# Performance work log

Hardware: AMD Instinct MI355X
Metric: run time of the kernel (lower is better)

The kernel has to match this reference:

```python
import jax, jax.numpy as jnp
import numpy as np

TARGET_MAIN_CONTRIBUTION = 0.6
CONTRIB_LOSS_COEF = 0.01
TOP_K = 2
NEG_INF = -1e9


def _gat(x, adj, W1, a1s, a1d, W2, a2s, a2d):
    """Dense 2-layer GAT (pyGAT style): multi-head concat + ELU, then one output head.
    x: [B,S,Fin], adj: [B,S,S], W1: [H,Fin,Fh], a1s/a1d: [H,Fh], W2: [H*Fh,Fout], a2s/a2d: [Fout]."""
    mask = adj > 0  # [B,S,S]
    h = jnp.einsum('bsf,hfo->bhso', x, W1)                      # [B,H,S,Fh]
    es = jnp.einsum('bhso,ho->bhs', h, a1s)
    ed = jnp.einsum('bhso,ho->bhs', h, a1d)
    e = jax.nn.leaky_relu(es[:, :, :, None] + ed[:, :, None, :], 0.2)  # [B,H,S,S]
    att = jax.nn.softmax(jnp.where(mask[:, None], e, NEG_INF), axis=-1)
    h1 = jax.nn.elu(jnp.einsum('bhst,bhto->bhso', att, h))      # [B,H,S,Fh]
    B, H, S, Fh = h1.shape
    h1 = h1.transpose(0, 2, 1, 3).reshape(B, S, H * Fh)         # concat heads
    h2 = h1 @ W2                                                # [B,S,Fout]
    e2 = jax.nn.leaky_relu((h2 @ a2s)[:, :, None] + (h2 @ a2d)[:, None, :], 0.2)
    att2 = jax.nn.softmax(jnp.where(mask, e2, NEG_INF), axis=-1)
    return jnp.einsum('bst,bto->bso', att2, h2)


def setup_inputs() -> dict:
    B, S, D, H, Hd, E = 4, 1024, 256, 6, 64, 3
    key = jax.random.key(0)
    ks = jax.random.split(key, 20)
    feature = jax.random.normal(ks[0], (B, S, D), dtype=jnp.float32)
    # sparse-ish binary adjacency with self-loops
    adj = (jax.random.uniform(ks[1], (B, S, S)) < 0.05).astype(jnp.float32)
    adj = jnp.maximum(adj, jnp.eye(S, dtype=jnp.float32)[None])
    p = lambda k, shape: jax.random.normal(k, shape, dtype=jnp.float32) * 0.1
    return {
        'feature': feature, 'adj': adj,
        'main_W1': p(ks[2], (H, D, Hd)), 'main_a1s': p(ks[3], (H, Hd)), 'main_a1d': p(ks[4], (H, Hd)),
        'main_W2': p(ks[5], (H * Hd, D)), 'main_a2s': p(ks[6], (D,)), 'main_a2d': p(ks[7], (D,)),
        'dep_W1': p(ks[8], (E, H, D, Hd)), 'dep_a1s': p(ks[9], (E, H, Hd)), 'dep_a1d': p(ks[10], (E, H, Hd)),
        'dep_W2': p(ks[11], (E, H * Hd, D)), 'dep_a2s': p(ks[12], (E, D)), 'dep_a2d': p(ks[13], (E, D)),
        'router_W': p(ks[14], (D, E)),
        'blend_W': p(ks[15], (D, D)), 'blend_b': jnp.zeros((D,), dtype=jnp.float32),
        'doc_num': 4, 'sect_num': 32,
    }


def reference(feature, adj, main_W1, main_a1s, main_a1d, main_W2, main_a2s, main_a2d,
              dep_W1, dep_a1s, dep_a1d, dep_W2, dep_a2s, dep_a2d,
              router_W, blend_W, blend_b, doc_num, sect_num):
    B, S, D = feature.shape
    E = router_W.shape[1]
    # main expert on full graph
    main_output = _gat(feature, adj, main_W1, main_a1s, main_a1d, main_W2, main_a2s, main_a2d)
    # per-expert adjacency views (zero out columns by node type)
    col = jnp.arange(S)
    sent_cols = (col < S - sect_num - doc_num).astype(adj.dtype)
    sect_cols = ((col >= S - sect_num - doc_num) & (col < S - doc_num)).astype(adj.dtype)
    doc_cols = (col >= S - doc_num).astype(adj.dtype)
    adj_stack = jnp.stack([adj * sent_cols, adj * sect_cols, adj * doc_cols])  # [E,B,S,S]
    # fixed top-k router
    x_flat = feature.reshape(-1, D)
    gate_probs = jax.nn.softmax(x_flat @ router_W, axis=-1)      # [B*S,E]
    _, top_idx = jax.lax.top_k(gate_probs, TOP_K)                # [B*S,k]
    routing_mask = jax.nn.one_hot(top_idx, E, dtype=feature.dtype).sum(axis=-2)  # [B*S,E] binary
    routing_mask = routing_mask.reshape(B, S, E)
    mask_e = routing_mask.transpose(2, 0, 1)[..., None]          # [E,B,S,1]
    # deputy experts: masked input, masked output, accumulate
    x_e = feature[None] * mask_e                                 # [E,B,S,D]
    dep_out = jax.vmap(_gat)(x_e, adj_stack, dep_W1, dep_a1s, dep_a1d, dep_W2, dep_a2s, dep_a2d)
    deputy_output = (dep_out * mask_e).sum(axis=0)               # [B,S,D]
    # blend gate
    blend_weight = jax.nn.sigmoid(feature @ blend_W + blend_b)
    final_output = blend_weight * main_output + (1.0 - blend_weight) * deputy_output
    main_contribution = blend_weight.mean()
    contribution_loss = jnp.abs(main_contribution - TARGET_MAIN_CONTRIBUTION) * CONTRIB_LOSS_COEF
    return final_output, contribution_loss, main_contribution
```

## Files before the change

kernel.cpp:

```cpp
#include <hip/hip_runtime.h>
#include <math.h>

#define B 4
#define S 1024
#define D 256
#define H 6
#define HD 64
#define NE 3
#define HHD 384
#define ROWS (B*S)
#define MAXN 128
#define PLN ((size_t)ROWS*64)

typedef __attribute__((ext_vector_type(8))) short bf8_t;
typedef __attribute__((ext_vector_type(4))) float f32x4;

__device__ __forceinline__ float leaky(float x){ return x > 0.f ? x : 0.2f*x; }

__device__ __forceinline__ unsigned short f2bf(float f){
    union { float f; unsigned int u; } v; v.f = f;
    unsigned int u = v.u;
    return (unsigned short)((u + 0x7FFFu + ((u >> 16) & 1u)) >> 16);
}
__device__ __forceinline__ float bf2f(unsigned short h){
    union { unsigned int u; float f; } v; v.u = ((unsigned int)h) << 16;
    return v.f;
}
__device__ __forceinline__ float blo(unsigned int u){
    union { unsigned int u; float f; } v; v.u = u << 16; return v.f;
}
__device__ __forceinline__ float bhi(unsigned int u){
    union { unsigned int u; float f; } v; v.u = u & 0xffff0000u; return v.f;
}
__device__ __forceinline__ float i2f(int t){
    union { int i; float f; } v; v.i = t; return v.f;
}
__device__ __forceinline__ int f2i(float f){
    union { float f; int i; } v; v.f = f; return v.i;
}
__device__ __forceinline__ unsigned int pk2(float lo, float hi){
    return (unsigned)f2bf(lo) | ((unsigned)f2bf(hi) << 16);
}

struct P {
    const float *feature, *adj;
    const float *main_W1, *dep_W1, *main_W2, *dep_W2, *blend_W, *router_W;
    const int *doc_p, *sect_p;
    const float *main_a1s, *main_a1d, *dep_a1s, *dep_a1d;
    const float *main_a2s, *main_a2d, *dep_a2s, *dep_a2d;
    const float *blend_b;
    unsigned short *featbf; short *nbr; int4 *nbc;
    unsigned short *w1nk, *w2nk, *bwt;
    float *es8, *ed8, *gatebuf;
    unsigned int *htp;
    unsigned short *h2n4, *h1c4;
    float *f2s4, *f2d4, *meanV1p, *meanV2, *sumBuf, *rmask;
    float *outp;
};

#define PB_CONV   1024
#define PB_NBR    1024
#define PB_W1     1536
#define PB_W2     1536
#define PB_BW      256
#define PB_ZERO    177
#define PB_ROUTER 1024
#define PB_TOTAL  (PB_CONV + PB_NBR + PB_W1 + PB_W2 + PB_BW + PB_ZERO + PB_ROUTER)
#define NZERO     45088

__global__ __launch_bounds__(256) void prep_kernel(P pp)
{
    int blk = blockIdx.x, tid = threadIdx.x;
    if (blk < PB_CONV){
        int idx = blk*256 + tid;
        float4 v = ((const float4*)pp.feature)[idx];
        ushort4 o;
        o.x = f2bf(v.x); o.y = f2bf(v.y); o.z = f2bf(v.z); o.w = f2bf(v.w);
        ((ushort4*)pp.featbf)[idx] = o;
        return;
    }
    blk -= PB_CONV;
    if (blk < PB_NBR){
        int wave = tid >> 6, lane = tid & 63;
        int row = blk*4 + wave;
        int b1 = S - *pp.sect_p - *pp.doc_p;
        int b2 = S - *pp.doc_p;
        const float* ar = pp.adj + (size_t)row*S + lane*16;
        float a[16];
        #pragma unroll
        for (int q = 0; q < 4; q++){
            float4 v = ((const float4*)ar)[q];
            a[q*4+0] = v.x; a[q*4+1] = v.y; a[q*4+2] = v.z; a[q*4+3] = v.w;
        }
        int t0 = lane*16;
        int k = 0, c1 = 0, c2 = 0;
        #pragma unroll
        for (int i = 0; i < 16; i++){
            if (a[i] > 0.f){
                k++;
                int t = t0 + i;
                if (t < b1) c1++;
                if (t < b2) c2++;
            }
        }
        int inc = k;
        #pragma unroll
        for (int d = 1; d < 64; d <<= 1){
            int u = __shfl_up(inc, d);
            if (lane >= d) inc += u;
        }
        int off = inc - k;
        int total = __shfl(inc, 63);
        int o = row*MAXN + off;
        #pragma unroll
        for (int i = 0; i < 16; i++){
            if (a[i] > 0.f) pp.nbr[o++] = (short)(t0 + i);
        }
        for (int d = 32; d; d >>= 1){
            c1 += __shfl_down(c1, d);
            c2 += __shfl_down(c2, d);
        }
        if (lane == 0) pp.nbc[row] = make_int4(total, c1, c2, 0);
        return;
    }
    blk -= PB_NBR;
    if (blk < PB_W1){
        int e = blk / 384;
        int idx = (blk - e*384)*256 + tid;
        const float* src = (e == 0) ? pp.main_W1 : pp.dep_W1 + (size_t)(e-1)*H*D*HD;
        int n = idx >> 8, k = idx & 255;
        int h = n >> 6, o = n & 63;
        pp.w1nk[(size_t)e*HHD*D + idx] = f2bf(src[(h*D + k)*HD + o]);
        return;
    }
    blk -= PB_W1;
    if (blk < PB_W2){
        int g = blk*256 + tid;
        int e = g / (D*HHD);
        int rem = g - e*(D*HHD);
        int n = rem / HHD, k = rem - n*HHD;
        const float* src = (e == 0) ? pp.main_W2 : pp.dep_W2 + (size_t)(e-1)*HHD*D;
        pp.w2nk[g] = f2bf(src[k*D + n]);
        return;
    }
    blk -= PB_W2;
    if (blk < PB_BW){
        int col = blk, k = tid;
        pp.bwt[col*D + k] = f2bf(pp.blend_W[k*D + col]);
        return;
    }
    blk -= PB_BW;
    if (blk < PB_ZERO){
        int idx = blk*256 + tid;
        if (idx < NZERO) pp.f2s4[idx] = 0.f;
        return;
    }
    blk -= PB_ZERO;
    {
        int wave = tid >> 6, lane = tid & 63;
        int row = blk*4 + wave;
        float4 xv = ((const float4*)(pp.feature + (size_t)row*D))[lane];
        int f = lane*4;
        float xa[4] = {xv.x, xv.y, xv.z, xv.w};
        float p0 = 0.f, p1 = 0.f, p2 = 0.f;
        #pragma unroll
        for (int j = 0; j < 4; j++){
            p0 += xa[j]*pp.router_W[(f+j)*NE + 0];
            p1 += xa[j]*pp.router_W[(f+j)*NE + 1];
            p2 += xa[j]*pp.router_W[(f+j)*NE + 2];
        }
        for (int off = 32; off; off >>= 1){
            p0 += __shfl_down(p0, off);
            p1 += __shfl_down(p1, off);
            p2 += __shfl_down(p2, off);
        }
        if (lane == 0){
            float p[3] = {p0, p1, p2};
            int ex = 0;
            for (int e = 1; e < NE; e++) if (p[e] <= p[ex]) ex = e;
            for (int e = 0; e < NE; e++) pp.rmask[e*ROWS + row] = (e == ex) ? 0.f : 1.f;
        }
    }
}

__global__ __launch_bounds__(256, 4) void gemm1_kernel(P pp)
{
    __shared__ __align__(16) char smem[17408];
    float (*ep)[2][64][17] = (float (*)[2][64][17])smem;
    unsigned int (*tile)[68] = (unsigned int (*)[68])smem;
    int tid = threadIdx.x, wave = tid >> 6, lane = tid & 63;
    int quad = lane >> 4, l16 = lane & 15;
    int e = blockIdx.z;
    int n0 = blockIdx.y*64;
    f32x4 z4 = {0.f,0.f,0.f,0.f};
    bf8_t bz = {0,0,0,0,0,0,0,0};

    if (e == 4){
        if (blockIdx.x >= 2) return;
        int m0 = blockIdx.x*128;
        const unsigned short* arow0 = pp.bwt + (size_t)(m0 + wave*16 + l16)*D + quad*8;
        const unsigned short* arow1 = arow0 + (size_t)64*D;
        const unsigned short* brow[4];
        #pragma unroll
        for (int j = 0; j < 4; j++)
            brow[j] = pp.featbf + (size_t)(n0 + j*16 + l16)*D + quad*8;
        f32x4 acc[8] = {z4, z4, z4, z4, z4, z4, z4, z4};
        bf8_t a0F = *(const bf8_t*)(arow0);
        bf8_t a1F = *(const bf8_t*)(arow1);
        bf8_t bF[4];
        #pragma unroll
        for (int j = 0; j < 4; j++) bF[j] = *(const bf8_t*)(brow[j]);
        #pragma unroll
        for (int it = 0; it < D/32; it++){
            bf8_t a0C = a0F, a1C = a1F;
            bf8_t bC[4] = {bF[0], bF[1], bF[2], bF[3]};
            if (it + 1 < D/32){
                int kn = (it + 1)*32;
                a0F = *(const bf8_t*)(arow0 + kn);
                a1F = *(const bf8_t*)(arow1 + kn);
                #pragma unroll
                for (int j = 0; j < 4; j++) bF[j] = *(const bf8_t*)(brow[j] + kn);
            }
            #pragma unroll
            for (int j = 0; j < 4; j++){
                acc[j]   = __builtin_amdgcn_mfma_f32_16x16x32_bf16(a0C, bC[j], acc[j],   0, 0, 0);
                acc[4+j] = __builtin_amdgcn_mfma_f32_16x16x32_bf16(a1C, bC[j], acc[4+j], 0, 0, 0);
            }
        }
        int mbase0 = m0 + wave*16 + quad*4;
        int mbase1 = mbase0 + 64;
        float bias0[4], bias1[4];
        #pragma unroll
        for (int r = 0; r < 4; r++){ bias0[r] = pp.blend_b[mbase0 + r]; bias1[r] = pp.blend_b[mbase1 + r]; }
        float lsum = 0.f;
        #pragma unroll
        for (int j = 0; j < 4; j++){
            int rown = n0 + j*16 + l16;
            f32x4 st0, st1;
            #pragma unroll
            for (int r = 0; r < 4; r++){
                float g0 = 1.f/(1.f + __expf(-(acc[j][r] + bias0[r])));
                float g1 = 1.f/(1.f + __expf(-(acc[4+j][r] + bias1[r])));
                lsum += g0 + g1;
                st0[r] = g0; st1[r] = g1;
            }
            *(f32x4*)(pp.gatebuf + (size_t)rown*D + mbase0) = st0;
            *(f32x4*)(pp.gatebuf + (size_t)rown*D + mbase1) = st1;
        }
        float* redp = (float*)smem;
        redp[tid] = lsum;
        __syncthreads();
        for (int sft = 128; sft; sft >>= 1){
            if (tid < sft) redp[tid] += redp[tid + sft];
            __syncthreads();
        }
        if (tid == 0) atomicAdd(pp.sumBuf, redp[0]);
        return;
    }

    int p = blockIdx.x;
    int m0 = p*128;
    const unsigned short* arow0 = pp.w1nk + (size_t)e*HHD*D + (size_t)(m0 + wave*16 + l16)*D + quad*8;
    const unsigned short* arow1 = arow0 + (size_t)64*D;
    const unsigned short* brow[4];
    bool zr[4];
    #pragma unroll
    for (int j = 0; j < 4; j++){
        int n = n0 + j*16 + l16;
        brow[j] = pp.featbf + (size_t)n*D + quad*8;
        zr[j] = (e > 0) ? (pp.rmask[(size_t)(e-1)*ROWS + n] == 0.f) : false;
    }
    f32x4 acc[8] = {z4, z4, z4, z4, z4, z4, z4, z4};
    bf8_t a0F = *(const bf8_t*)(arow0);
    bf8_t a1F = *(const bf8_t*)(arow1);
    bf8_t bF[4];
    #pragma unroll
    for (int j = 0; j < 4; j++) bF[j] = zr[j] ? bz : *(const bf8_t*)(brow[j]);
    #pragma unroll
    for (int it = 0; it < D/32; it++){
        bf8_t a0C = a0F, a1C = a1F;
        bf8_t bC[4] = {bF[0], bF[1], bF[2], bF[3]};
        if (it + 1 < D/32){
            int kn = (it + 1)*32;
            a0F = *(const bf8_t*)(arow0 + kn);
            a1F = *(const bf8_t*)(arow1 + kn);
            #pragma unroll
            for (int j = 0; j < 4; j++) bF[j] = zr[j] ? bz : *(const bf8_t*)(brow[j] + kn);
        }
        #pragma unroll
        for (int j = 0; j < 4; j++){
            acc[j]   = __builtin_amdgcn_mfma_f32_16x16x32_bf16(a0C, bC[j], acc[j],   0, 0, 0);
            acc[4+j] = __builtin_amdgcn_mfma_f32_16x16x32_bf16(a1C, bC[j], acc[4+j], 0, 0, 0);
        }
    }
    int b = n0 >> 10;
    int mbase0 = m0 + wave*16 + quad*4;
    int mbase1 = mbase0 + 64;
    int obase = wave*16 + quad*4;
    int h0 = p*2, h1 = p*2 + 1;
    const float* a1sp = (e == 0) ? pp.main_a1s : pp.dep_a1s + (size_t)(e-1)*H*HD;
    const float* a1dp = (e == 0) ? pp.main_a1d : pp.dep_a1d + (size_t)(e-1)*H*HD;
    float s0v[4], d0v[4], s1v[4], d1v[4];
    #pragma unroll
    for (int r = 0; r < 4; r++){
        s0v[r] = a1sp[mbase0 + r]; d0v[r] = a1dp[mbase0 + r];
        s1v[r] = a1sp[mbase1 + r]; d1v[r] = a1dp[mbase1 + r];
    }
    #pragma unroll
    for (int j = 0; j < 4; j++){
        float ps0 = 0.f, pd0 = 0.f, ps1 = 0.f, pd1 = 0.f;
        #pragma unroll
        for (int r = 0; r < 4; r++){
            ps0 += acc[j][r]*s0v[r];   pd0 += acc[j][r]*d0v[r];
            ps1 += acc[4+j][r]*s1v[r]; pd1 += acc[4+j][r]*d1v[r];
        }
        ep[0][0][j*16 + l16][wave*4 + quad] = ps0;
        ep[0][1][j*16 + l16][wave*4 + quad] = pd0;
        ep[1][0][j*16 + l16][wave*4 + quad] = ps1;
        ep[1][1][j*16 + l16][wave*4 + quad] = pd1;
    }
    float* mvb = pp.meanV1p + ((size_t)e*B + b)*512;
    #pragma unroll
    for (int r = 0; r < 4; r++){
        float cm0 = acc[0][r] + acc[1][r] + acc[2][r] + acc[3][r];
        float cm1 = acc[4][r] + acc[5][r] + acc[6][r] + acc[7][r];
        for (int off = 8; off; off >>= 1){
            cm0 += __shfl_down(cm0, off, 16);
            cm1 += __shfl_down(cm1, off, 16);
        }
        if (l16 == 0){
            atomicAdd(mvb + (obase + r)*8 + h0, cm0*(1.f/(float)S));
            atomicAdd(mvb + (obase + r)*8 + h1, cm1*(1.f/(float)S));
        }
    }
    __syncthreads();
    {
        int hh = tid >> 7, arr = (tid >> 6) & 1, sl = tid & 63;
        float sum = 0.f;
        #pragma unroll
        for (int i = 0; i < 16; i++) sum += ep[hh][arr][sl][i];
        int n = n0 + sl;
        float* dst = arr ? pp.ed8 : pp.es8;
        dst[(((size_t)e*B + (n >> 10))*S + (n & 1023))*8 + (p*2 + hh)] = sum;
    }
    __syncthreads();
    #pragma unroll
    for (int j = 0; j < 4; j++){
        int rloc = j*16 + l16;
        tile[rloc][obase + 0] = pk2(acc[j][0], acc[4+j][0]);
        tile[rloc][obase + 1] = pk2(acc[j][1], acc[4+j][1]);
        tile[rloc][obase + 2] = pk2(acc[j][2], acc[4+j][2]);
        tile[rloc][obase + 3] = pk2(acc[j][3], acc[4+j][3]);
    }
    __syncthreads();
    {
        unsigned int* plane = pp.htp + (size_t)(e*3 + p)*PLN;
        int o4 = (tid & 15)*4;
        int rsub = tid >> 4;
        #pragma unroll
        for (int pass = 0; pass < 4; pass++){
            int rloc = pass*16 + rsub;
            uint4 v = *(const uint4*)&tile[rloc][o4];
            *(uint4*)(plane + (size_t)(n0 + rloc)*64 + o4) = v;
        }
    }
}

__global__ __launch_bounds__(256) void a1_kernel(P pp)
{
    __shared__ f32x4 wMa[MAXN], wMb[MAXN], wDa[MAXN], wDb[MAXN];
    __shared__ f32x4 paccA[4][64], paccB[4][64];
    __shared__ float pdenM[2][6];
    __shared__ float pdenD[2][3][6];
    int tid = threadIdx.x, wave = tid >> 6, lane = tid & 63;
    int s = blockIdx.x, b = blockIdx.y;
    int row = b*S + s;
    int4 c = pp.nbc[row];
    const short* nl = pp.nbr + (size_t)row*MAXN;

    if (wave < 2){
        const float* esp = pp.es8 + ((size_t)b*S + s)*8;
        f32x4 eslo = *(const f32x4*)esp;
        f32x4 eshi = *(const f32x4*)(esp + 4);
        float esv[6] = {eslo[0], eslo[1], eslo[2], eslo[3], eshi[0], eshi[1]};
        const float* edb = pp.ed8 + (size_t)b*S*8;
        int i = wave*64 + lane;
        float w[6] = {0,0,0,0,0,0};
        if (i < c.x){
            int t = nl[i];
            const float* epn = edb + (size_t)t*8;
            f32x4 d0 = *(const f32x4*)epn;
            f32x4 d1 = *(const f32x4*)(epn + 4);
            float edv[6] = {d0[0], d0[1], d0[2], d0[3], d1[0], d1[1]};
            #pragma unroll
            for (int h = 0; h < 6; h++) w[h] = __expf(leaky(esv[h] + edv[h]));
            f32x4 ra = {w[0], w[1], w[2], w[3]};
            f32x4 rb = {w[4], w[5], i2f(t), 0.f};
            wMa[i] = ra; wMb[i] = rb;
        }
        #pragma unroll
        for (int h = 0; h < 6; h++){
            float x = w[h];
            for (int o2 = 32; o2; o2 >>= 1) x += __shfl_down(x, o2);
            if (lane == 0) pdenM[wave][h] = x;
        }
    } else {
        int i = (wave - 2)*64 + lane;
        int tg = (i < c.y) ? 1 : ((i < c.z) ? 2 : 3);
        float w[6] = {0,0,0,0,0,0};
        if (i < c.x){
            int t = nl[i];
            const float* esp = pp.es8 + (((size_t)tg*B + b)*S + s)*8;
            f32x4 eslo = *(const f32x4*)esp;
            f32x4 eshi = *(const f32x4*)(esp + 4);
            const float* epn = pp.ed8 + (((size_t)tg*B + b)*S + (size_t)t)*8;
            f32x4 d0 = *(const f32x4*)epn;
            f32x4 d1 = *(const f32x4*)(epn + 4);
            float es6[6] = {eslo[0], eslo[1], eslo[2], eslo[3], eshi[0], eshi[1]};
            float ed6[6] = {d0[0], d0[1], d0[2], d0[3], d1[0], d1[1]};
            #pragma unroll
            for (int h = 0; h < 6; h++) w[h] = __expf(leaky(es6[h] + ed6[h]));
            float zf = (pp.rmask[(size_t)(tg-1)*ROWS + (size_t)b*S + t] == 0.f) ? 1.f : 0.f;
            f32x4 ra = {w[0], w[1], w[2], w[3]};
            f32x4 rb = {w[4], w[5], zf, 0.f};
            wDa[i] = ra; wDb[i] = rb;
        }
        #pragma unroll
        for (int g = 1; g <= 3; g++){
            #pragma unroll
            for (int h = 0; h < 6; h++){
                float x = (tg == g) ? w[h] : 0.f;
                for (int o2 = 32; o2; o2 >>= 1) x += __shfl_down(x, o2);
                if (lane == 0) pdenD[wave-2][g-1][h] = x;
            }
        }
    }
    __syncthreads();

    const unsigned int* Vm = pp.htp + (size_t)b*S*64 + lane;
    float accM[6] = {0,0,0,0,0,0};
    int rlo[3] = {0, c.y, c.z};
    int rhi[3] = {c.y, c.z, c.x};
    for (int rg = 0; rg < 3; rg++){
        const unsigned int* Vd = pp.htp + (size_t)(rg+1)*3*PLN + (size_t)b*S*64 + lane;
        float accD[6] = {0,0,0,0,0,0};
        #pragma unroll 2
        for (int j = rlo[rg] + wave; j < rhi[rg]; j += 4){
            f32x4 ma = wMa[j], mb = wMb[j];
            f32x4 da = wDa[j], db = wDb[j];
            size_t toff = (size_t)f2i(mb[2])*64;
            unsigned int u0 = Vm[toff];
            unsigned int u1 = Vm[toff + PLN];
            unsigned int u2 = Vm[toff + 2*PLN];
            accM[0] += ma[0]*blo(u0); accM[1] += ma[1]*bhi(u0);
            accM[2] += ma[2]*blo(u1); accM[3] += ma[3]*bhi(u1);
            accM[4] += mb[0]*blo(u2); accM[5] += mb[1]*bhi(u2);
            if (db[2] == 0.f){
                unsigned int d0 = Vd[toff];
                unsigned int d1 = Vd[toff + PLN];
                unsigned int d2 = Vd[toff + 2*PLN];
                accD[0] += da[0]*blo(d0); accD[1] += da[1]*bhi(d0);
                accD[2] += da[2]*blo(d1); accD[3] += da[3]*bhi(d1);
                accD[4] += db[0]*blo(d2); accD[5] += db[1]*bhi(d2);
            }
        }
        {
            f32x4 pa = {accD[0], accD[1], accD[2], accD[3]};
            f32x4 pb = {accD[4], accD[5], 0.f, 0.f};
            paccA[wave][lane] = pa; paccB[wave][lane] = pb;
        }
        __syncthreads();
        if (wave == 0){
            unsigned short* outp = pp.h1c4 + ((size_t)(rg+1)*ROWS + row)*HHD;
            bool has = rhi[rg] > rlo[rg];
            const float* mv = pp.meanV1p + ((size_t)(rg+1)*B + b)*512 + lane*8;
            f32x4 q0 = paccA[0][lane], q1 = paccA[1][lane], q2 = paccA[2][lane], q3 = paccA[3][lane];
            f32x4 r0 = paccB[0][lane], r1 = paccB[1][lane], r2 = paccB[2][lane], r3 = paccB[3][lane];
            float sum6[6];
            sum6[0] = q0[0]+q1[0]+q2[0]+q3[0];
            sum6[1] = q0[1]+q1[1]+q2[1]+q3[1];
            sum6[2] = q0[2]+q1[2]+q2[2]+q3[2];
            sum6[3] = q0[3]+q1[3]+q2[3]+q3[3];
            sum6[4] = r0[0]+r1[0]+r2[0]+r3[0];
            sum6[5] = r0[1]+r1[1]+r2[1]+r3[1];
            #pragma unroll
            for (int h = 0; h < 6; h++){
                float den = pdenD[0][rg][h] + pdenD[1][rg][h];
                float v = has ? sum6[h]/den : mv[h];
                v = v > 0.f ? v : __expf(v) - 1.f;
                outp[h*64 + lane] = f2bf(v);
            }
        }
        __syncthreads();
    }
    {
        f32x4 pa = {accM[0], accM[1], accM[2], accM[3]};
        f32x4 pb = {accM[4], accM[5], 0.f, 0.f};
        paccA[wave][lane] = pa; paccB[wave][lane] = pb;
    }
    __syncthreads();
    if (wave == 0){
        unsigned short* outp = pp.h1c4 + (size_t)row*HHD;
        f32x4 q0 = paccA[0][lane], q1 = paccA[1][lane], q2 = paccA[2][lane], q3 = paccA[3][lane];
        f32x4 r0 = paccB[0][lane], r1 = paccB[1][lane], r2 = paccB[2][lane], r3 = paccB[3][lane];
        float sum6[6];
        sum6[0] = q0[0]+q1[0]+q2[0]+q3[0];
        sum6[1] = q0[1]+q1[1]+q2[1]+q3[1];
        sum6[2] = q0[2]+q1[2]+q2[2]+q3[2];
        sum6[3] = q0[3]+q1[3]+q2[3]+q3[3];
        sum6[4] = r0[0]+r1[0]+r2[0]+r3[0];
        sum6[5] = r0[1]+r1[1]+r2[1]+r3[1];
        #pragma unroll
        for (int h = 0; h < 6; h++){
            float den = pdenM[0][h] + pdenM[1][h];
            float v = sum6[h]/den;
            v = v > 0.f ? v : __expf(v) - 1.f;
            outp[h*64 + lane] = f2bf(v);
        }
    }
}

__global__ __launch_bounds__(256, 4) void gemm2_kernel(P pp)
{
    __shared__ float ep[2][2][64][17];
    int tid = threadIdx.x, wave = tid >> 6, lane = tid & 63;
    int quad = lane >> 4, l16 = lane & 15;
    int e = blockIdx.z;
    int m0 = blockIdx.x*128;
    int n0 = blockIdx.y*64;
    f32x4 z4 = {0.f,0.f,0.f,0.f};
    const unsigned short* arow0 = pp.w2nk + (size_t)e*D*HHD + (size_t)(m0 + wave*16 + l16)*HHD + quad*8;
    const unsigned short* arow1 = arow0 + (size_t)64*HHD;
    const unsigned short* brow[4];
    #pragma unroll
    for (int j = 0; j < 4; j++)
        brow[j] = pp.h1c4 + (size_t)e*ROWS*HHD + (size_t)(n0 + j*16 + l16)*HHD + quad*8;
    f32x4 acc[8] = {z4, z4, z4, z4, z4, z4, z4, z4};
    bf8_t a0F = *(const bf8_t*)(arow0);
    bf8_t a1F = *(const bf8_t*)(arow1);
    bf8_t bF[4];
    #pragma unroll
    for (int j = 0; j < 4; j++) bF[j] = *(const bf8_t*)(brow[j]);
    #pragma unroll
    for (int it = 0; it < HHD/32; it++){
        bf8_t a0C = a0F, a1C = a1F;
        bf8_t bC[4] = {bF[0], bF[1], bF[2], bF[3]};
        if (it + 1 < HHD/32){
            int kn = (it + 1)*32;
            a0F = *(const bf8_t*)(arow0 + kn);
            a1F = *(const bf8_t*)(arow1 + kn);
            #pragma unroll
            for (int j = 0; j < 4; j++) bF[j] = *(const bf8_t*)(brow[j] + kn);
        }
        #pragma unroll
        for (int j = 0; j < 4; j++){
            acc[j]   = __builtin_amdgcn_mfma_f32_16x16x32_bf16(a0C, bC[j], acc[j],   0, 0, 0);
            acc[4+j] = __builtin_amdgcn_mfma_f32_16x16x32_bf16(a1C, bC[j], acc[4+j], 0, 0, 0);
        }
    }
    int b = n0 >> 10;
    int mbase0 = m0 + wave*16 + quad*4;
    int mbase1 = mbase0 + 64;
    #pragma unroll
    for (int j = 0; j < 4; j++){
        int row = n0 + j*16 + l16;
        ushort4 o0, o1;
        o0.x = f2bf(acc[j][0]);   o0.y = f2bf(acc[j][1]);
        o0.z = f2bf(acc[j][2]);   o0.w = f2bf(acc[j][3]);
        o1.x = f2bf(acc[4+j][0]); o1.y = f2bf(acc[4+j][1]);
        o1.z = f2bf(acc[4+j][2]); o1.w = f2bf(acc[4+j][3]);
        *(ushort4*)(pp.h2n4 + ((size_t)e*ROWS + row)*D + mbase0) = o0;
        *(ushort4*)(pp.h2n4 + ((size_t)e*ROWS + row)*D + mbase1) = o1;
    }
    const float* a2sp = (e == 0) ? pp.main_a2s : pp.dep_a2s + (size_t)(e-1)*D;
    const float* a2dp = (e == 0) ? pp.main_a2d : pp.dep_a2d + (size_t)(e-1)*D;
    float s0v[4], d0v[4], s1v[4], d1v[4];
    #pragma unroll
    for (int r = 0; r < 4; r++){
        s0v[r] = a2sp[mbase0 + r]; d0v[r] = a2dp[mbase0 + r];
        s1v[r] = a2sp[mbase1 + r]; d1v[r] = a2dp[mbase1 + r];
    }
    #pragma unroll
    for (int j = 0; j < 4; j++){
        float ps0 = 0.f, pd0 = 0.f, ps1 = 0.f, pd1 = 0.f;
        #pragma unroll
        for (int r = 0; r < 4; r++){
            ps0 += acc[j][r]*s0v[r];   pd0 += acc[j][r]*d0v[r];
            ps1 += acc[4+j][r]*s1v[r]; pd1 += acc[4+j][r]*d1v[r];
        }
        ep[0][0][j*16 + l16][wave*4 + quad] = ps0;
        ep[0][1][j*16 + l16][wave*4 + quad] = pd0;
        ep[1][0][j*16 + l16][wave*4 + quad] = ps1;
        ep[1][1][j*16 + l16][wave*4 + quad] = pd1;
    }
    #pragma unroll
    for (int r = 0; r < 4; r++){
        float cm0 = acc[0][r] + acc[1][r] + acc[2][r] + acc[3][r];
        float cm1 = acc[4][r] + acc[5][r] + acc[6][r] + acc[7][r];
        for (int off = 8; off; off >>= 1){
            cm0 += __shfl_down(cm0, off, 16);
            cm1 += __shfl_down(cm1, off, 16);
        }
        if (l16 == 0){
            atomicAdd(pp.meanV2 + ((size_t)e*B + b)*D + mbase0 + r, cm0*(1.f/(float)S));
            atomicAdd(pp.meanV2 + ((size_t)e*B + b)*D + mbase1 + r, cm1*(1.f/(float)S));
        }
    }
    __syncthreads();
    {
        int hh = tid >> 7, arr = (tid >> 6) & 1, sl = tid & 63;
        float sum = 0.f;
        #pragma unroll
        for (int i = 0; i < 16; i++) sum += ep[hh][arr][sl][i];
        int n = n0 + sl;
        float* dst = arr ? pp.f2d4 : pp.f2s4;
        atomicAdd(dst + (size_t)e*ROWS + n, sum);
    }
}

__global__ __launch_bounds__(256) void a2_kernel(P pp)
{
    __shared__ float2 wrec0[MAXN];
    __shared__ float2 wrec1[MAXN];
    __shared__ float pacc[3][256];
    __shared__ float pden[4][4];
    int tid = threadIdx.x;
    int wave = tid >> 6, lane = tid & 63;
    int s = blockIdx.x, b = blockIdx.y;
    int row = b*S + s;
    int4 c = pp.nbc[row];
    float rm0 = pp.rmask[row], rm1 = pp.rmask[ROWS + row], rm2 = pp.rmask[2*ROWS + row];
    const short* nl = pp.nbr + (size_t)row*MAXN;
    if (wave < 2){
        int i = wave*64 + lane;
        float w = 0.f;
        if (i < c.x){
            int t = nl[i];
            float fs = pp.f2s4[row];
            w = __expf(leaky(fs + pp.f2d4[(size_t)b*S + t]));
            float2 r; r.x = w; r.y = i2f(t);
            wrec0[i] = r;
        }
        float dsum = w;
        for (int o2 = 32; o2; o2 >>= 1) dsum += __shfl_down(dsum, o2);
        if (lane == 0) pden[wave][0] = dsum;
    } else {
        int i = (wave - 2)*64 + lane;
        float w = 0.f, d1 = 0.f, d2 = 0.f, d3 = 0.f;
        if (i < c.x){
            int t = nl[i];
            int tag = (i < c.y) ? 1 : ((i < c.z) ? 2 : 3);
            float act = (tag == 1) ? rm0 : ((tag == 2) ? rm1 : rm2);
            if (act != 0.f){
                float fs = pp.f2s4[(size_t)tag*ROWS + row];
                w = __expf(leaky(fs + pp.f2d4[(size_t)tag*ROWS + (size_t)b*S + t]));
            }
            float2 r; r.x = w; r.y = i2f(t);
            wrec1[i] = r;
            if (tag == 1) d1 = w; else if (tag == 2) d2 = w; else d3 = w;
        }
        for (int o2 = 32; o2; o2 >>= 1){
            d1 += __shfl_down(d1, o2);
            d2 += __shfl_down(d2, o2);
            d3 += __shfl_down(d3, o2);
        }
        if (lane == 0){ pden[wave][1] = d1; pden[wave][2] = d2; pden[wave][3] = d3; }
    }
    __syncthreads();
    float acc[4] = {0.f, 0.f, 0.f, 0.f};
    if (wave < 2){
        float inv = 1.f/(pden[0][0] + pden[1][0]);
        const unsigned short* V = pp.h2n4 + (size_t)b*S*D;
        #pragma unroll 4
        for (int j = wave; j < c.x; j += 2){
            float2 r = wrec0[j];
            float wv = r.x*inv;
            int t = f2i(r.y);
            const unsigned short* vp = V + (size_t)t*D + lane*4;
            uint2 dv = *(const uint2*)vp;
            acc[0] += wv*blo(dv.x); acc[1] += wv*bhi(dv.x);
            acc[2] += wv*blo(dv.y); acc[3] += wv*bhi(dv.y);
        }
    } else {
        int rlo[3] = {0, c.y, c.z};
        int rhi[3] = {c.y, c.z, c.x};
        float ract[3] = {rm0, rm1, rm2};
        for (int rg = 0; rg < 3; rg++){
            if (ract[rg] == 0.f || rhi[rg] <= rlo[rg]) continue;
            float inv = 1.f/(pden[2][rg+1] + pden[3][rg+1]);
            const unsigned short* V = pp.h2n4 + ((size_t)(rg+1)*ROWS + (size_t)b*S)*D;
            #pragma unroll 4
            for (int j = rlo[rg] + (wave - 2); j < rhi[rg]; j += 2){
                float2 r = wrec1[j];
                float wv = r.x*inv;
                int t = f2i(r.y);
                const unsigned short* vp = V + (size_t)t*D + lane*4;
                uint2 dv = *(const uint2*)vp;
                acc[0] += wv*blo(dv.x); acc[1] += wv*bhi(dv.x);
                acc[2] += wv*blo(dv.y); acc[3] += wv*bhi(dv.y);
            }
        }
    }
    if (wave >= 1){
        #pragma unroll
        for (int q = 0; q < 4; q++) pacc[wave-1][lane*4 + q] = acc[q];
    }
    __syncthreads();
    if (wave == 0){
        float4 g4 = *(const float4*)(pp.gatebuf + (size_t)row*D + lane*4);
        float dep_mv[4] = {0.f, 0.f, 0.f, 0.f};
        if (rm0 != 0.f && c.y == 0){
            float4 mv = *(const float4*)(pp.meanV2 + ((size_t)1*B + b)*D + lane*4);
            dep_mv[0] += mv.x; dep_mv[1] += mv.y; dep_mv[2] += mv.z; dep_mv[3] += mv.w;
        }
        if (rm1 != 0.f && c.z == c.y){
            float4 mv = *(const float4*)(pp.meanV2 + ((size_t)2*B + b)*D + lane*4);
            dep_mv[0] += mv.x; dep_mv[1] += mv.y; dep_mv[2] += mv.z; dep_mv[3] += mv.w;
        }
        if (rm2 != 0.f && c.x == c.z){
            float4 mv = *(const float4*)(pp.meanV2 + ((size_t)3*B + b)*D + lane*4);
            dep_mv[0] += mv.x; dep_mv[1] += mv.y; dep_mv[2] += mv.z; dep_mv[3] += mv.w;
        }
        float g[4] = {g4.x, g4.y, g4.z, g4.w};
        float4 o;
        float* op = &o.x;
        #pragma unroll
        for (int q = 0; q < 4; q++){
            int col = lane*4 + q;
            float a0 = acc[q] + pacc[0][col];
            float dep = pacc[1][col] + pacc[2][col] + dep_mv[q];
            op[q] = g[q]*a0 + (1.f - g[q])*dep;
        }
        *(float4*)(pp.outp + (size_t)row*D + lane*4) = o;
    }
    if (blockIdx.x == 0 && blockIdx.y == 0 && tid == 0){
        float mc = pp.sumBuf[0] / (float)(ROWS*D);
        pp.outp[ROWS*D]     = fabsf(mc - 0.6f)*0.01f;
        pp.outp[ROWS*D + 1] = mc;
    }
}

extern "C" void kernel_launch(void* const* d_in, const int* in_sizes, int n_in,
                              void* d_out, int out_size, void* d_ws, size_t ws_size,
                              hipStream_t stream)
{
    P hp;
    hp.feature  = (const float*)d_in[0];
    hp.adj      = (const float*)d_in[1];
    hp.main_W1  = (const float*)d_in[2];
    hp.main_a1s = (const float*)d_in[3];
    hp.main_a1d = (const float*)d_in[4];
    hp.main_W2  = (const float*)d_in[5];
    hp.main_a2s = (const float*)d_in[6];
    hp.main_a2d = (const float*)d_in[7];
    hp.dep_W1   = (const float*)d_in[8];
    hp.dep_a1s  = (const float*)d_in[9];
    hp.dep_a1d  = (const float*)d_in[10];
    hp.dep_W2   = (const float*)d_in[11];
    hp.dep_a2s  = (const float*)d_in[12];
    hp.dep_a2d  = (const float*)d_in[13];
    hp.router_W = (const float*)d_in[14];
    hp.blend_W  = (const float*)d_in[15];
    hp.blend_b  = (const float*)d_in[16];
    hp.doc_p    = (const int*)d_in[17];
    hp.sect_p   = (const int*)d_in[18];

    char* ws = (char*)d_ws;
    size_t off = 0;
    hp.featbf = (unsigned short*)(ws + off); off += (size_t)ROWS*D*2;
    hp.nbr    = (short*)(ws + off);          off += (size_t)ROWS*MAXN*2;
    hp.nbc    = (int4*)(ws + off);           off += (size_t)ROWS*16;
    hp.w1nk   = (unsigned short*)(ws + off); off += (size_t)4*HHD*D*2;
    hp.w2nk   = (unsigned short*)(ws + off); off += (size_t)4*D*HHD*2;
    hp.bwt    = (unsigned short*)(ws + off); off += (size_t)D*D*2;
    hp.es8 = (float*)(ws + off); off += (size_t)4*B*S*8*4;
    hp.ed8 = (float*)(ws + off); off += (size_t)4*B*S*8*4;
    hp.gatebuf = (float*)(ws + off); off += (size_t)ROWS*D*4;
    hp.htp  = (unsigned int*)(ws + off);     off += (size_t)12*PLN*4;
    hp.h2n4 = (unsigned short*)(ws + off); off += (size_t)4*ROWS*D*2;
    hp.h1c4 = (unsigned short*)(ws + off); off += (size_t)4*ROWS*HHD*2;
    hp.f2s4    = (float*)(ws + off); off += (size_t)4*ROWS*4;
    hp.f2d4    = (float*)(ws + off); off += (size_t)4*ROWS*4;
    hp.meanV1p = (float*)(ws + off); off += (size_t)4*B*512*4;
    hp.meanV2  = (float*)(ws + off); off += (size_t)4*B*D*4;
    hp.sumBuf  = (float*)(ws + off); off += 128;
    hp.rmask   = (float*)(ws + off); off += (size_t)NE*ROWS*4;
    hp.outp    = (float*)d_out;

    prep_kernel<<<PB_TOTAL, 256, 0, stream>>>(hp);
    gemm1_kernel<<<dim3(3, ROWS/64, 5), 256, 0, stream>>>(hp);
    a1_kernel<<<dim3(S, B), 256, 0, stream>>>(hp);
    gemm2_kernel<<<dim3(D/128, ROWS/64, 4), 256, 0, stream>>>(hp);
    a2_kernel<<<dim3(S, B), 256, 0, stream>>>(hp);
}
```

Before: 221.5 us.

## Interleave per-head value planes and prefetch neighbor gathers in attention kernels

Adds a small kernel that repacks the three separate bf16 value planes into one interleaved 16-byte record per row. The first-layer aggregation can then fetch each neighbor with a single vector load instead of three scattered loads. The main and deputy gather loops in a1 and a2 are rewritten with explicit one-step software prefetch. The per-neighbor routing-mask check is dropped, and blocks are remapped linearly so neighbouring blocks cover several batches. The extra repack pass costs added memory traffic and workspace, and dropping the mask check assumes masked rows already hold zero values.

```diff
diff --git a/kernel.cpp b/kernel.cpp
--- a/kernel.cpp
+++ b/kernel.cpp
@@ -53,6 +53,7 @@
     unsigned short *w1nk, *w2nk, *bwt;
     float *es8, *ed8, *gatebuf;
     unsigned int *htp;
+    unsigned int *hti;
     unsigned short *h2n4, *h1c4;
     float *f2s4, *f2d4, *meanV1p, *meanV2, *sumBuf, *rmask;
     float *outp;
@@ -366,6 +367,20 @@
     }
 }
 
+__global__ __launch_bounds__(256) void ilv_kernel(P pp)
+{
+    int e = blockIdx.x >> 10;
+    int row = (blockIdx.x & 1023)*4 + (threadIdx.x >> 6);
+    int o = threadIdx.x & 63;
+    const unsigned int* src = pp.htp + (size_t)e*3*PLN + (size_t)row*64 + o;
+    uint4 v;
+    v.x = src[0];
+    v.y = src[PLN];
+    v.z = src[2*PLN];
+    v.w = 0u;
+    *(uint4*)(pp.hti + ((size_t)e*ROWS + row)*256 + o*4) = v;
+}
+
 __global__ __launch_bounds__(256) void a1_kernel(P pp)
 {
     __shared__ f32x4 wMa[MAXN], wMb[MAXN], wDa[MAXN], wDb[MAXN];
@@ -373,7 +388,9 @@
     __shared__ float pdenM[2][6];
     __shared__ float pdenD[2][3][6];
     int tid = threadIdx.x, wave = tid >> 6, lane = tid & 63;
-    int s = blockIdx.x, b = blockIdx.y;
+    int lin = blockIdx.x;
+    int b = (lin & 7) >> 1;
+    int s = (lin >> 3)*2 + (lin & 1);
     int row = b*S + s;
     int4 c = pp.nbc[row];
     const short* nl = pp.nbr + (size_t)row*MAXN;
@@ -420,9 +437,8 @@
             float ed6[6] = {d0[0], d0[1], d0[2], d0[3], d1[0], d1[1]};
             #pragma unroll
             for (int h = 0; h < 6; h++) w[h] = __expf(leaky(es6[h] + ed6[h]));
-            float zf = (pp.rmask[(size_t)(tg-1)*ROWS + (size_t)b*S + t] == 0.f) ? 1.f : 0.f;
             f32x4 ra = {w[0], w[1], w[2], w[3]};
-            f32x4 rb = {w[4], w[5], zf, 0.f};
+            f32x4 rb = {w[4], w[5], 0.f, 0.f};
             wDa[i] = ra; wDb[i] = rb;
         }
         #pragma unroll
@@ -437,32 +453,39 @@
     }
     __syncthreads();
 
-    const unsigned int* Vm = pp.htp + (size_t)b*S*64 + lane;
+    const unsigned int* Vm = pp.hti + (size_t)b*S*256 + lane*4;
     float accM[6] = {0,0,0,0,0,0};
     int rlo[3] = {0, c.y, c.z};
     int rhi[3] = {c.y, c.z, c.x};
     for (int rg = 0; rg < 3; rg++){
-        const unsigned int* Vd = pp.htp + (size_t)(rg+1)*3*PLN + (size_t)b*S*64 + lane;
+        const unsigned int* Vd = pp.hti + ((size_t)(rg+1)*ROWS + (size_t)b*S)*256 + lane*4;
         float accD[6] = {0,0,0,0,0,0};
-        #pragma unroll 2
-        for (int j = rlo[rg] + wave; j < rhi[rg]; j += 4){
-            f32x4 ma = wMa[j], mb = wMb[j];
-            f32x4 da = wDa[j], db = wDb[j];
-            size_t toff = (size_t)f2i(mb[2])*64;
-            unsigned int u0 = Vm[toff];
-            unsigned int u1 = Vm[toff + PLN];
-            unsigned int u2 = Vm[toff + 2*PLN];
-            accM[0] += ma[0]*blo(u0); accM[1] += ma[1]*bhi(u0);
-            accM[2] += ma[2]*blo(u1); accM[3] += ma[3]*bhi(u1);
-            accM[4] += mb[0]*blo(u2); accM[5] += mb[1]*bhi(u2);
-            if (db[2] == 0.f){
-                unsigned int d0 = Vd[toff];
-                unsigned int d1 = Vd[toff + PLN];
-                unsigned int d2 = Vd[toff + 2*PLN];
-                accD[0] += da[0]*blo(d0); accD[1] += da[1]*bhi(d0);
-                accD[2] += da[2]*blo(d1); accD[3] += da[3]*bhi(d1);
-                accD[4] += db[0]*blo(d2); accD[5] += db[1]*bhi(d2);
-            }
+        int j = rlo[rg] + wave, jend = rhi[rg];
+        f32x4 ma = {0,0,0,0}, mb = {0,0,0,0}, da = {0,0,0,0}, db = {0,0,0,0};
+        uint4 um = {0,0,0,0}, ud = {0,0,0,0};
+        if (j < jend){
+            ma = wMa[j]; mb = wMb[j]; da = wDa[j]; db = wDb[j];
+            size_t toff = (size_t)f2i(mb[2])*256;
+            um = *(const uint4*)(Vm + toff);
+            ud = *(const uint4*)(Vd + toff);
+        }
+        while (j < jend){
+            f32x4 cma = ma, cmb = mb, cda = da, cdb = db;
+            uint4 cum = um, cud = ud;
+            int jn = j + 4;
+            if (jn < jend){
+                ma = wMa[jn]; mb = wMb[jn]; da = wDa[jn]; db = wDb[jn];
+                size_t toff = (size_t)f2i(mb[2])*256;
+                um = *(const uint4*)(Vm + toff);
+                ud = *(const uint4*)(Vd + toff);
+            }
+            accM[0] += cma[0]*blo(cum.x); accM[1] += cma[1]*bhi(cum.x);
+            accM[2] += cma[2]*blo(cum.y); accM[3] += cma[3]*bhi(cum.y);
+            accM[4] += cmb[0]*blo(cum.z); accM[5] += cmb[1]*bhi(cum.z);
+            accD[0] += cda[0]*blo(cud.x); accD[1] += cda[1]*bhi(cud.x);
+            accD[2] += cda[2]*blo(cud.y); accD[3] += cda[3]*bhi(cud.y);
+            accD[4] += cdb[0]*blo(cud.z); accD[5] += cdb[1]*bhi(cud.z);
+            j = jn;
         }
         {
             f32x4 pa = {accD[0], accD[1], accD[2], accD[3]};
@@ -626,7 +649,9 @@
     __shared__ float pden[4][4];
     int tid = threadIdx.x;
     int wave = tid >> 6, lane = tid & 63;
-    int s = blockIdx.x, b = blockIdx.y;
+    int lin = blockIdx.x;
+    int b = (lin & 7) >> 1;
+    int s = (lin >> 3)*2 + (lin & 1);
     int row = b*S + s;
     int4 c = pp.nbc[row];
     float rm0 = pp.rmask[row], rm1 = pp.rmask[ROWS + row], rm2 = pp.rmask[2*ROWS + row];
@@ -671,15 +696,23 @@
     if (wave < 2){
         float inv = 1.f/(pden[0][0] + pden[1][0]);
         const unsigned short* V = pp.h2n4 + (size_t)b*S*D;
-        #pragma unroll 4
-        for (int j = wave; j < c.x; j += 2){
-            float2 r = wrec0[j];
-            float wv = r.x*inv;
-            int t = f2i(r.y);
-            const unsigned short* vp = V + (size_t)t*D + lane*4;
-            uint2 dv = *(const uint2*)vp;
-            acc[0] += wv*blo(dv.x); acc[1] += wv*bhi(dv.x);
-            acc[2] += wv*blo(dv.y); acc[3] += wv*bhi(dv.y);
+        int j = wave;
+        float2 rn = {0.f, 0.f}; uint2 un = {0u, 0u};
+        if (j < c.x){
+            rn = wrec0[j];
+            un = *(const uint2*)(V + (size_t)f2i(rn.y)*D + lane*4);
+        }
+        while (j < c.x){
+            float2 rc = rn; uint2 uc = un;
+            int jn = j + 2;
+            if (jn < c.x){
+                rn = wrec0[jn];
+                un = *(const uint2*)(V + (size_t)f2i(rn.y)*D + lane*4);
+            }
+            float wv = rc.x*inv;
+            acc[0] += wv*blo(uc.x); acc[1] += wv*bhi(uc.x);
+            acc[2] += wv*blo(uc.y); acc[3] += wv*bhi(uc.y);
+            j = jn;
         }
     } else {
         int rlo[3] = {0, c.y, c.z};
@@ -689,15 +722,23 @@
             if (ract[rg] == 0.f || rhi[rg] <= rlo[rg]) continue;
             float inv = 1.f/(pden[2][rg+1] + pden[3][rg+1]);
             const unsigned short* V = pp.h2n4 + ((size_t)(rg+1)*ROWS + (size_t)b*S)*D;
-            #pragma unroll 4
-            for (int j = rlo[rg] + (wave - 2); j < rhi[rg]; j += 2){
-                float2 r = wrec1[j];
-                float wv = r.x*inv;
-                int t = f2i(r.y);
-                const unsigned short* vp = V + (size_t)t*D + lane*4;
-                uint2 dv = *(const uint2*)vp;
-                acc[0] += wv*blo(dv.x); acc[1] += wv*bhi(dv.x);
-                acc[2] += wv*blo(dv.y); acc[3] += wv*bhi(dv.y);
+            int j = rlo[rg] + (wave - 2), jend = rhi[rg];
+            float2 rn = {0.f, 0.f}; uint2 un = {0u, 0u};
+            if (j < jend){
+                rn = wrec1[j];
+                un = *(const uint2*)(V + (size_t)f2i(rn.y)*D + lane*4);
+            }
+            while (j < jend){
+                float2 rc = rn; uint2 uc = un;
+                int jn = j + 2;
+                if (jn < jend){
+                    rn = wrec1[jn];
+                    un = *(const uint2*)(V + (size_t)f2i(rn.y)*D + lane*4);
+                }
+                float wv = rc.x*inv;
+                acc[0] += wv*blo(uc.x); acc[1] += wv*bhi(uc.x);
+                acc[2] += wv*blo(uc.y); acc[3] += wv*bhi(uc.y);
+                j = jn;
             }
         }
     }
@@ -733,7 +774,7 @@
         }
         *(float4*)(pp.outp + (size_t)row*D + lane*4) = o;
     }
-    if (blockIdx.x == 0 && blockIdx.y == 0 && tid == 0){
+    if (lin == 0 && tid == 0){
         float mc = pp.sumBuf[0] / (float)(ROWS*D);
         pp.outp[ROWS*D]     = fabsf(mc - 0.6f)*0.01f;
         pp.outp[ROWS*D + 1] = mc;
@@ -777,6 +818,7 @@
     hp.ed8 = (float*)(ws + off); off += (size_t)4*B*S*8*4;
     hp.gatebuf = (float*)(ws + off); off += (size_t)ROWS*D*4;
     hp.htp  = (unsigned int*)(ws + off);     off += (size_t)12*PLN*4;
+    hp.hti  = (unsigned int*)(ws + off);     off += (size_t)4*ROWS*256*4;
     hp.h2n4 = (unsigned short*)(ws + off); off += (size_t)4*ROWS*D*2;
     hp.h1c4 = (unsigned short*)(ws + off); off += (size_t)4*ROWS*HHD*2;
     hp.f2s4    = (float*)(ws + off); off += (size_t)4*ROWS*4;
@@ -789,7 +831,8 @@
 
     prep_kernel<<<PB_TOTAL, 256, 0, stream>>>(hp);
     gemm1_kernel<<<dim3(3, ROWS/64, 5), 256, 0, stream>>>(hp);
-    a1_kernel<<<dim3(S, B), 256, 0, stream>>>(hp);
+    ilv_kernel<<<4096, 256, 0, stream>>>(hp);
+    a1_kernel<<<4096, 256, 0, stream>>>(hp);
     gemm2_kernel<<<dim3(D/128, ROWS/64, 4), 256, 0, stream>>>(hp);
-    a2_kernel<<<dim3(S, B), 256, 0, stream>>>(hp);
-}
+    a2_kernel<<<4096, 256, 0, stream>>>(hp);
+}
```

After: 240.8 us. 8.7% more time.

## Interleave head planes into uint4 rows and widen attention kernel to 8 waves

Applied to the files above, without the earlier changes.

Adds an interleave kernel that repacks the three bf16 head-pair planes of each node into one 16-byte record, so the layer-1 neighbour gather issues a single vector load per neighbour instead of three strided scalar loads. The aggregation kernel also moves to 512 threads, with 8 waves striding the neighbour list, to expose more parallel gathers. In exchange there is an extra kernel launch and an extra pass writing a padded copy (one unused word per record), plus larger shared reduction buffers.

```diff
diff --git a/kernel.cpp b/kernel.cpp
--- a/kernel.cpp
+++ b/kernel.cpp
@@ -53,6 +53,7 @@
     unsigned short *w1nk, *w2nk, *bwt;
     float *es8, *ed8, *gatebuf;
     unsigned int *htp;
+    unsigned int *hti;
     unsigned short *h2n4, *h1c4;
     float *f2s4, *f2d4, *meanV1p, *meanV2, *sumBuf, *rmask;
     float *outp;
@@ -366,10 +367,24 @@
     }
 }
 
-__global__ __launch_bounds__(256) void a1_kernel(P pp)
+__global__ __launch_bounds__(256) void ilv_kernel(P pp)
+{
+    int e = blockIdx.x >> 10;
+    int row = (blockIdx.x & 1023)*4 + (threadIdx.x >> 6);
+    int o = threadIdx.x & 63;
+    const unsigned int* src = pp.htp + (size_t)e*3*PLN + (size_t)row*64 + o;
+    uint4 v;
+    v.x = src[0];
+    v.y = src[PLN];
+    v.z = src[2*PLN];
+    v.w = 0u;
+    *(uint4*)(pp.hti + ((size_t)e*ROWS + row)*256 + o*4) = v;
+}
+
+__global__ __launch_bounds__(512) void a1_kernel(P pp)
 {
     __shared__ f32x4 wMa[MAXN], wMb[MAXN], wDa[MAXN], wDb[MAXN];
-    __shared__ f32x4 paccA[4][64], paccB[4][64];
+    __shared__ f32x4 paccA[8][64], paccB[8][64];
     __shared__ float pdenM[2][6];
     __shared__ float pdenD[2][3][6];
     int tid = threadIdx.x, wave = tid >> 6, lane = tid & 63;
@@ -404,7 +419,7 @@
             for (int o2 = 32; o2; o2 >>= 1) x += __shfl_down(x, o2);
             if (lane == 0) pdenM[wave][h] = x;
         }
-    } else {
+    } else if (wave < 4){
         int i = (wave - 2)*64 + lane;
         int tg = (i < c.y) ? 1 : ((i < c.z) ? 2 : 3);
         float w[6] = {0,0,0,0,0,0};
@@ -437,31 +452,27 @@
     }
     __syncthreads();
 
-    const unsigned int* Vm = pp.htp + (size_t)b*S*64 + lane;
+    const unsigned int* Vm = pp.hti + (size_t)b*S*256 + lane*4;
     float accM[6] = {0,0,0,0,0,0};
     int rlo[3] = {0, c.y, c.z};
     int rhi[3] = {c.y, c.z, c.x};
     for (int rg = 0; rg < 3; rg++){
-        const unsigned int* Vd = pp.htp + (size_t)(rg+1)*3*PLN + (size_t)b*S*64 + lane;
+        const unsigned int* Vd = pp.hti + ((size_t)(rg+1)*ROWS + (size_t)b*S)*256 + lane*4;
         float accD[6] = {0,0,0,0,0,0};
         #pragma unroll 2
-        for (int j = rlo[rg] + wave; j < rhi[rg]; j += 4){
+        for (int j = rlo[rg] + wave; j < rhi[rg]; j += 8){
             f32x4 ma = wMa[j], mb = wMb[j];
             f32x4 da = wDa[j], db = wDb[j];
-            size_t toff = (size_t)f2i(mb[2])*64;
-            unsigned int u0 = Vm[toff];
-            unsigned int u1 = Vm[toff + PLN];
-            unsigned int u2 = Vm[toff + 2*PLN];
-            accM[0] += ma[0]*blo(u0); accM[1] += ma[1]*bhi(u0);
-            accM[2] += ma[2]*blo(u1); accM[3] += ma[3]*bhi(u1);
-            accM[4] += mb[0]*blo(u2); accM[5] += mb[1]*bhi(u2);
+            size_t toff = (size_t)f2i(mb[2])*256;
+            uint4 vm = *(const uint4*)(Vm + toff);
+            accM[0] += ma[0]*blo(vm.x); accM[1] += ma[1]*bhi(vm.x);
+            accM[2] += ma[2]*blo(vm.y); accM[3] += ma[3]*bhi(vm.y);
+            accM[4] += mb[0]*blo(vm.z); accM[5] += mb[1]*bhi(vm.z);
             if (db[2] == 0.f){
-                unsigned int d0 = Vd[toff];
-                unsigned int d1 = Vd[toff + PLN];
-                unsigned int d2 = Vd[toff + 2*PLN];
-                accD[0] += da[0]*blo(d0); accD[1] += da[1]*bhi(d0);
-                accD[2] += da[2]*blo(d1); accD[3] += da[3]*bhi(d1);
-                accD[4] += db[0]*blo(d2); accD[5] += db[1]*bhi(d2);
+                uint4 vd = *(const uint4*)(Vd + toff);
+                accD[0] += da[0]*blo(vd.x); accD[1] += da[1]*bhi(vd.x);
+                accD[2] += da[2]*blo(vd.y); accD[3] += da[3]*bhi(vd.y);
+                accD[4] += db[0]*blo(vd.z); accD[5] += db[1]*bhi(vd.z);
             }
         }
         {
@@ -474,15 +485,13 @@
             unsigned short* outp = pp.h1c4 + ((size_t)(rg+1)*ROWS + row)*HHD;
             bool has = rhi[rg] > rlo[rg];
             const float* mv = pp.meanV1p + ((size_t)(rg+1)*B + b)*512 + lane*8;
-            f32x4 q0 = paccA[0][lane], q1 = paccA[1][lane], q2 = paccA[2][lane], q3 = paccA[3][lane];
-            f32x4 r0 = paccB[0][lane], r1 = paccB[1][lane], r2 = paccB[2][lane], r3 = paccB[3][lane];
-            float sum6[6];
-            sum6[0] = q0[0]+q1[0]+q2[0]+q3[0];
-            sum6[1] = q0[1]+q1[1]+q2[1]+q3[1];
-            sum6[2] = q0[2]+q1[2]+q2[2]+q3[2];
-            sum6[3] = q0[3]+q1[3]+q2[3]+q3[3];
-            sum6[4] = r0[0]+r1[0]+r2[0]+r3[0];
-            sum6[5] = r0[1]+r1[1]+r2[1]+r3[1];
+            float sum6[6] = {0,0,0,0,0,0};
+            #pragma unroll
+            for (int wv2 = 0; wv2 < 8; wv2++){
+                f32x4 qa = paccA[wv2][lane], qb = paccB[wv2][lane];
+                sum6[0] += qa[0]; sum6[1] += qa[1]; sum6[2] += qa[2];
+                sum6[3] += qa[3]; sum6[4] += qb[0]; sum6[5] += qb[1];
+            }
             #pragma unroll
             for (int h = 0; h < 6; h++){
                 float den = pdenD[0][rg][h] + pdenD[1][rg][h];
@@ -501,15 +510,13 @@
     __syncthreads();
     if (wave == 0){
         unsigned short* outp = pp.h1c4 + (size_t)row*HHD;
-        f32x4 q0 = paccA[0][lane], q1 = paccA[1][lane], q2 = paccA[2][lane], q3 = paccA[3][lane];
-        f32x4 r0 = paccB[0][lane], r1 = paccB[1][lane], r2 = paccB[2][lane], r3 = paccB[3][lane];
-        float sum6[6];
-        sum6[0] = q0[0]+q1[0]+q2[0]+q3[0];
-        sum6[1] = q0[1]+q1[1]+q2[1]+q3[1];
-        sum6[2] = q0[2]+q1[2]+q2[2]+q3[2];
-        sum6[3] = q0[3]+q1[3]+q2[3]+q3[3];
-        sum6[4] = r0[0]+r1[0]+r2[0]+r3[0];
-        sum6[5] = r0[1]+r1[1]+r2[1]+r3[1];
+        float sum6[6] = {0,0,0,0,0,0};
+        #pragma unroll
+        for (int wv2 = 0; wv2 < 8; wv2++){
+            f32x4 qa = paccA[wv2][lane], qb = paccB[wv2][lane];
+            sum6[0] += qa[0]; sum6[1] += qa[1]; sum6[2] += qa[2];
+            sum6[3] += qa[3]; sum6[4] += qb[0]; sum6[5] += qb[1];
+        }
         #pragma unroll
         for (int h = 0; h < 6; h++){
             float den = pdenM[0][h] + pdenM[1][h];
@@ -777,6 +784,7 @@
     hp.ed8 = (float*)(ws + off); off += (size_t)4*B*S*8*4;
     hp.gatebuf = (float*)(ws + off); off += (size_t)ROWS*D*4;
     hp.htp  = (unsigned int*)(ws + off);     off += (size_t)12*PLN*4;
+    hp.hti  = (unsigned int*)(ws + off);     off += (size_t)4*ROWS*256*4;
     hp.h2n4 = (unsigned short*)(ws + off); off += (size_t)4*ROWS*D*2;
     hp.h1c4 = (unsigned short*)(ws + off); off += (size_t)4*ROWS*HHD*2;
     hp.f2s4    = (float*)(ws + off); off += (size_t)4*ROWS*4;
@@ -789,7 +797,8 @@
 
     prep_kernel<<<PB_TOTAL, 256, 0, stream>>>(hp);
     gemm1_kernel<<<dim3(3, ROWS/64, 5), 256, 0, stream>>>(hp);
-    a1_kernel<<<dim3(S, B), 256, 0, stream>>>(hp);
+    ilv_kernel<<<4096, 256, 0, stream>>>(hp);
+    a1_kernel<<<dim3(S, B), 512, 0, stream>>>(hp);
     gemm2_kernel<<<dim3(D/128, ROWS/64, 4), 256, 0, stream>>>(hp);
     a2_kernel<<<dim3(S, B), 256, 0, stream>>>(hp);
 }
```

After: 260.6 us. 17.6% more time.

## Interleave head planes for single 16-byte gathers in layer-1 attention aggregation

Applied to the files above, without the earlier changes.

Adds an interleave kernel that copies the three per-head bf16 planes of the layer-1 projections into one layout with a 16-byte record per node and lane. The neighbour-aggregation loop then issues one vector load per neighbour instead of three scattered 4-byte loads. The loop also drops the per-neighbour routing-mask lookup and branch and always accumulates the deputy contribution, relying on masked rows already being zero. In exchange, the extra kernel adds a full read and write of the projection buffers and a new workspace allocation, and the deputy path now loads data for every neighbour.

```diff
diff --git a/kernel.cpp b/kernel.cpp
--- a/kernel.cpp
+++ b/kernel.cpp
@@ -53,6 +53,7 @@
     unsigned short *w1nk, *w2nk, *bwt;
     float *es8, *ed8, *gatebuf;
     unsigned int *htp;
+    unsigned int *hti;
     unsigned short *h2n4, *h1c4;
     float *f2s4, *f2d4, *meanV1p, *meanV2, *sumBuf, *rmask;
     float *outp;
@@ -364,6 +365,20 @@
             *(uint4*)(plane + (size_t)(n0 + rloc)*64 + o4) = v;
         }
     }
+}
+
+__global__ __launch_bounds__(256) void ilv_kernel(P pp)
+{
+    int e = blockIdx.x >> 10;
+    int row = (blockIdx.x & 1023)*4 + (threadIdx.x >> 6);
+    int o = threadIdx.x & 63;
+    const unsigned int* src = pp.htp + (size_t)e*3*PLN + (size_t)row*64 + o;
+    uint4 v;
+    v.x = src[0];
+    v.y = src[PLN];
+    v.z = src[2*PLN];
+    v.w = 0u;
+    *(uint4*)(pp.hti + ((size_t)e*ROWS + row)*256 + o*4) = v;
 }
 
 __global__ __launch_bounds__(256) void a1_kernel(P pp)
@@ -420,9 +435,8 @@
             float ed6[6] = {d0[0], d0[1], d0[2], d0[3], d1[0], d1[1]};
             #pragma unroll
             for (int h = 0; h < 6; h++) w[h] = __expf(leaky(es6[h] + ed6[h]));
-            float zf = (pp.rmask[(size_t)(tg-1)*ROWS + (size_t)b*S + t] == 0.f) ? 1.f : 0.f;
             f32x4 ra = {w[0], w[1], w[2], w[3]};
-            f32x4 rb = {w[4], w[5], zf, 0.f};
+            f32x4 rb = {w[4], w[5], 0.f, 0.f};
             wDa[i] = ra; wDb[i] = rb;
         }
         #pragma unroll
@@ -437,32 +451,26 @@
     }
     __syncthreads();
 
-    const unsigned int* Vm = pp.htp + (size_t)b*S*64 + lane;
+    const unsigned int* Vm = pp.hti + (size_t)b*S*256 + lane*4;
     float accM[6] = {0,0,0,0,0,0};
     int rlo[3] = {0, c.y, c.z};
     int rhi[3] = {c.y, c.z, c.x};
     for (int rg = 0; rg < 3; rg++){
-        const unsigned int* Vd = pp.htp + (size_t)(rg+1)*3*PLN + (size_t)b*S*64 + lane;
+        const unsigned int* Vd = pp.hti + ((size_t)(rg+1)*ROWS + (size_t)b*S)*256 + lane*4;
         float accD[6] = {0,0,0,0,0,0};
         #pragma unroll 2
         for (int j = rlo[rg] + wave; j < rhi[rg]; j += 4){
             f32x4 ma = wMa[j], mb = wMb[j];
             f32x4 da = wDa[j], db = wDb[j];
-            size_t toff = (size_t)f2i(mb[2])*64;
-            unsigned int u0 = Vm[toff];
-            unsigned int u1 = Vm[toff + PLN];
-            unsigned int u2 = Vm[toff + 2*PLN];
-            accM[0] += ma[0]*blo(u0); accM[1] += ma[1]*bhi(u0);
-            accM[2] += ma[2]*blo(u1); accM[3] += ma[3]*bhi(u1);
-            accM[4] += mb[0]*blo(u2); accM[5] += mb[1]*bhi(u2);
-            if (db[2] == 0.f){
-                unsigned int d0 = Vd[toff];
-                unsigned int d1 = Vd[toff + PLN];
-                unsigned int d2 = Vd[toff + 2*PLN];
-                accD[0] += da[0]*blo(d0); accD[1] += da[1]*bhi(d0);
-                accD[2] += da[2]*blo(d1); accD[3] += da[3]*bhi(d1);
-                accD[4] += db[0]*blo(d2); accD[5] += db[1]*bhi(d2);
-            }
+            size_t toff = (size_t)f2i(mb[2])*256;
+            uint4 vm = *(const uint4*)(Vm + toff);
+            uint4 vd = *(const uint4*)(Vd + toff);
+            accM[0] += ma[0]*blo(vm.x); accM[1] += ma[1]*bhi(vm.x);
+            accM[2] += ma[2]*blo(vm.y); accM[3] += ma[3]*bhi(vm.y);
+            accM[4] += mb[0]*blo(vm.z); accM[5] += mb[1]*bhi(vm.z);
+            accD[0] += da[0]*blo(vd.x); accD[1] += da[1]*bhi(vd.x);
+            accD[2] += da[2]*blo(vd.y); accD[3] += da[3]*bhi(vd.y);
+            accD[4] += db[0]*blo(vd.z); accD[5] += db[1]*bhi(vd.z);
         }
         {
             f32x4 pa = {accD[0], accD[1], accD[2], accD[3]};
@@ -777,6 +785,7 @@
     hp.ed8 = (float*)(ws + off); off += (size_t)4*B*S*8*4;
     hp.gatebuf = (float*)(ws + off); off += (size_t)ROWS*D*4;
     hp.htp  = (unsigned int*)(ws + off);     off += (size_t)12*PLN*4;
+    hp.hti  = (unsigned int*)(ws + off);     off += (size_t)4*ROWS*256*4;
     hp.h2n4 = (unsigned short*)(ws + off); off += (size_t)4*ROWS*D*2;
     hp.h1c4 = (unsigned short*)(ws + off); off += (size_t)4*ROWS*HHD*2;
     hp.f2s4    = (float*)(ws + off); off += (size_t)4*ROWS*4;
@@ -789,6 +798,7 @@
 
     prep_kernel<<<PB_TOTAL, 256, 0, stream>>>(hp);
     gemm1_kernel<<<dim3(3, ROWS/64, 5), 256, 0, stream>>>(hp);
+    ilv_kernel<<<4096, 256, 0, stream>>>(hp);
     a1_kernel<<<dim3(S, B), 256, 0, stream>>>(hp);
     gemm2_kernel<<<dim3(D/128, ROWS/64, 4), 256, 0, stream>>>(hp);
     a2_kernel<<<dim3(S, B), 256, 0, stream>>>(hp);
```

Result: slower. 228.3 us (+3.1%).
